# Kernel optimization log

Hardware: AMD Instinct MI355X
Metric: run time of the kernel (lower is better)

Reference implementation:

```python
import jax, jax.numpy as jnp
import numpy as np
import math

D_MODEL = 1024
N_HEAD = 16
D_HEAD = D_MODEL // N_HEAD


def setup_inputs() -> dict:
    key = jax.random.key(0)
    k0, k1, k2, k3, k4 = jax.random.split(key, 5)
    B, N = 4, 2048
    inp = jax.random.normal(k0, (B, N, D_MODEL), dtype=jnp.float32)
    # causal mask: True = keep (masked_fill on ~mask)
    mask = jnp.tril(jnp.ones((N, N), dtype=bool))
    # qkv_proj Linear(d_model, 3*d_model); output Linear(d_model, d_model)
    s_in = 1.0 / math.sqrt(D_MODEL)
    W_qkv = jax.random.uniform(k1, (D_MODEL, 3 * D_MODEL), jnp.float32, -s_in, s_in)
    b_qkv = jax.random.uniform(k2, (3 * D_MODEL,), jnp.float32, -s_in, s_in)
    W_out = jax.random.uniform(k3, (D_MODEL, D_MODEL), jnp.float32, -s_in, s_in)
    b_out = jax.random.uniform(k4, (D_MODEL,), jnp.float32, -s_in, s_in)
    return {"input": inp, "W_qkv": W_qkv, "b_qkv": b_qkv,
            "W_out": W_out, "b_out": b_out, "mask": mask}


def reference(input, W_qkv, b_qkv, W_out, b_out, mask):
    B, N, d = input.shape
    qkv = input @ W_qkv + b_qkv                       # [B,N,3d]  (dropout=eval no-op)
    q, k, v = jnp.split(qkv, 3, axis=-1)
    # [B,N,H,Dh] -> [B,H,N,Dh]
    q = q.reshape(B, N, N_HEAD, D_HEAD).transpose(0, 2, 1, 3)
    k = k.reshape(B, N, N_HEAD, D_HEAD).transpose(0, 2, 1, 3)
    v = v.reshape(B, N, N_HEAD, D_HEAD).transpose(0, 2, 1, 3)
    scale = 1.0 / math.sqrt(D_HEAD)
    scores = jnp.einsum('bhqd,bhkd->bhqk', q, k) * scale   # [B,H,N,N]
    scores = jnp.where(mask, scores, -jnp.inf)
    attn = jax.nn.softmax(scores, axis=-1)
    out = jnp.einsum('bhqk,bhkd->bhqd', attn, v)           # [B,H,N,Dh]
    out = out.transpose(0, 2, 1, 3).reshape(B, N, d)       # concat heads
    return out @ W_out + b_out
```

## Files before the change

kernel.cpp:

```cpp
#include <hip/hip_runtime.h>
#include <hip/hip_bf16.h>

typedef unsigned short u16;
typedef unsigned u32;
typedef __attribute__((ext_vector_type(4))) unsigned short u16x4;
typedef __attribute__((ext_vector_type(8))) unsigned short u16x8;
typedef __attribute__((ext_vector_type(4))) unsigned u32x4;
typedef __attribute__((ext_vector_type(8))) __bf16 bf16x8;
typedef __attribute__((ext_vector_type(4))) float f32x4;

typedef __attribute__((address_space(1))) void as1v;
typedef __attribute__((address_space(3))) void as3v;

#define MFMA16(a, b, c) __builtin_amdgcn_mfma_f32_16x16x32_bf16(a, b, c, 0, 0, 0)

__device__ __forceinline__ u16 f2bf(float f) {
    unsigned u = __builtin_bit_cast(unsigned, f);
    u += 0x7fffu + ((u >> 16) & 1u);
    return (u16)(u >> 16);
}

__device__ __forceinline__ u32 pkbf(float lo, float hi) {
    u32 r;
    asm("v_cvt_pk_bf16_f32 %0, %1, %2" : "=v"(r) : "v"(lo), "v"(hi));
    return r;
}

__device__ __forceinline__ void gload16(const void* g, void* l) {
    __builtin_amdgcn_global_load_lds((as1v*)g, (as3v*)l, 16, 0, 0);
}

__global__ void convert_f32_bf16(const float* __restrict__ in, u16* __restrict__ out, int n4) {
    int i = blockIdx.x * blockDim.x + threadIdx.x;
    if (i < n4) {
        float4 v = *(const float4*)&in[(size_t)i * 4];
        u16x4 o;
        o.x = f2bf(v.x); o.y = f2bf(v.y); o.z = f2bf(v.z); o.w = f2bf(v.w);
        *(u16x4*)&out[(size_t)i * 4] = o;
    }
}

__global__ void transpose_convert(const float* __restrict__ in, u16* __restrict__ out, int R, int C) {
    __shared__ float tl[64][65];
    const int rb = blockIdx.x, cb = blockIdx.y;
    const int tid = threadIdx.x;
    for (int it = 0; it < 4; ++it) {
        int lin = (tid + it * 256) * 4;
        int r = lin >> 6, c = lin & 63;
        float4 v = *(const float4*)&in[(size_t)(rb * 64 + r) * C + cb * 64 + c];
        tl[r][c + 0] = v.x; tl[r][c + 1] = v.y; tl[r][c + 2] = v.z; tl[r][c + 3] = v.w;
    }
    __syncthreads();
    for (int it = 0; it < 4; ++it) {
        int lin = (tid + it * 256) * 4;
        int oc = lin >> 6, orr = lin & 63;
        u16x4 o;
        o.x = f2bf(tl[orr + 0][oc]);
        o.y = f2bf(tl[orr + 1][oc]);
        o.z = f2bf(tl[orr + 2][oc]);
        o.w = f2bf(tl[orr + 3][oc]);
        *(u16x4*)&out[(size_t)(cb * 64 + oc) * R + rb * 64 + orr] = o;
    }
}

__global__ void transpose_v(const u16* __restrict__ vbuf, u16* __restrict__ vtb) {
    __shared__ u16 tl[64][65];
    const int nb = blockIdx.x, bh = blockIdx.y;
    const int tid = threadIdx.x;
    for (int it = 0; it < 2; ++it) {
        int lin = (tid + it * 256) * 8;
        int nl = lin >> 6, dh = lin & 63;
        u16x8 v = *(const u16x8*)&vbuf[((size_t)bh * 2048 + nb * 64 + nl) * 64 + dh];
#pragma unroll
        for (int j = 0; j < 8; ++j) tl[dh + j][nl] = v[j];
    }
    __syncthreads();
    for (int it = 0; it < 2; ++it) {
        int lin = (tid + it * 256) * 8;
        int dh = lin >> 6, nl = lin & 63;
        u16x8 o;
#pragma unroll
        for (int j = 0; j < 8; ++j) o[j] = tl[dh][nl + j];
        *(u16x8*)&vtb[((size_t)bh * 64 + dh) * 2048 + nb * 64 + nl] = o;
    }
}

__global__ __launch_bounds__(512, 2) void gemm256_qkv(
    const u16* __restrict__ A, const u16* __restrict__ Bt, const float* __restrict__ bias,
    u16* __restrict__ qb, u16* __restrict__ kb, u16* __restrict__ vb) {
    constexpr int K = 1024;
    constexpr int NT = 32;
    __shared__ u16 ldsu[65536];

    const int bid = blockIdx.x;
    const int swz = (bid & 7) * 48 + (bid >> 3);
    const int bm = swz / 12, bn = swz % 12;

    const int tid = threadIdx.x, wid = tid >> 6, lane = tid & 63;
    const int wr = wid >> 2, wc = wid & 3;
    const int l15 = lane & 15, lhi = lane >> 4;

    const int sslot = (lane & 7) ^ (lane >> 3);
    const int kcol = (sslot & 3) * 8;
    const int mloc = (lane >> 3) * 2 + (sslot >> 2);

    const u16* Arow[2];
    const u16* Brow[2];
#pragma unroll
    for (int li = 0; li < 2; ++li) {
        int sg = wid * 2 + li;
        int m = sg * 16 + mloc;
        Arow[li] = A + (size_t)(bm * 256 + m) * K + kcol;
        Brow[li] = Bt + (size_t)(bn * 256 + m) * K + kcol;
    }

    auto stageA = [&](int buf, int t) {
#pragma unroll
        for (int li = 0; li < 2; ++li) {
            int sg = wid * 2 + li;
            gload16(Arow[li] + t * 32, (char*)ldsu + buf * 32768 + sg * 1024);
        }
    };
    auto stageB = [&](int buf, int t) {
#pragma unroll
        for (int li = 0; li < 2; ++li) {
            int sg = wid * 2 + li;
            gload16(Brow[li] + t * 32, (char*)ldsu + buf * 32768 + 16384 + sg * 1024);
        }
    };

    const int rslot = ((l15 & 1) * 4 + lhi) ^ ((l15 >> 1) & 7);
    const int fragoff = (l15 >> 1) * 64 + rslot * 8;

    f32x4 acc[8][4];
#pragma unroll
    for (int i = 0; i < 8; ++i)
#pragma unroll
        for (int j = 0; j < 4; ++j) acc[i][j] = (f32x4){0.f, 0.f, 0.f, 0.f};

    auto doTile = [&](int cur, int tstage, bool dostage) {
        const u16* Ab = ldsu + cur * 16384 + wr * 4096 + fragoff;
        const u16* Bb = ldsu + cur * 16384 + 8192 + wc * 2048 + fragoff;
        bf16x8 af[8], b0, b1;
#pragma unroll
        for (int mf = 0; mf < 8; ++mf) af[mf] = *(const bf16x8*)(Ab + mf * 512);
        b0 = *(const bf16x8*)(Bb);
        b1 = *(const bf16x8*)(Bb + 512);
        if (dostage) stageA(tstage & 3, tstage);
        __builtin_amdgcn_s_setprio(1);
#pragma unroll
        for (int mf = 0; mf < 8; ++mf) {
            acc[mf][0] = MFMA16(af[mf], b0, acc[mf][0]);
            acc[mf][1] = MFMA16(af[mf], b1, acc[mf][1]);
        }
        __builtin_amdgcn_s_setprio(0);
        b0 = *(const bf16x8*)(Bb + 1024);
        b1 = *(const bf16x8*)(Bb + 1536);
        if (dostage) stageB(tstage & 3, tstage);
        __builtin_amdgcn_s_setprio(1);
#pragma unroll
        for (int mf = 0; mf < 8; ++mf) {
            acc[mf][2] = MFMA16(af[mf], b0, acc[mf][2]);
            acc[mf][3] = MFMA16(af[mf], b1, acc[mf][3]);
        }
        __builtin_amdgcn_s_setprio(0);
    };

    stageA(0, 0); stageB(0, 0);
    stageA(1, 1); stageB(1, 1);
    stageA(2, 2); stageB(2, 2);
    asm volatile("s_waitcnt vmcnt(8)" ::: "memory");
    __builtin_amdgcn_s_barrier();
    __builtin_amdgcn_sched_barrier(0);

    for (int t = 0; t < NT - 3; ++t) {
        doTile(t & 3, t + 3, true);
        asm volatile("s_waitcnt vmcnt(8)" ::: "memory");
        __builtin_amdgcn_s_barrier();
        __builtin_amdgcn_sched_barrier(0);
    }
    doTile((NT - 3) & 3, 0, false);
    asm volatile("s_waitcnt vmcnt(4)" ::: "memory");
    __builtin_amdgcn_s_barrier();
    __builtin_amdgcn_sched_barrier(0);
    doTile((NT - 2) & 3, 0, false);
    asm volatile("s_waitcnt vmcnt(0)" ::: "memory");
    __builtin_amdgcn_s_barrier();
    __builtin_amdgcn_sched_barrier(0);
    doTile((NT - 1) & 3, 0, false);

    const int bnbase = bn * 256 + wc * 64;
#pragma unroll
    for (int nf = 0; nf < 4; ++nf) {
        int cg = bnbase + nf * 16 + l15;
        float bv = bias[cg];
        int which = cg >> 10, rem = cg & 1023;
        u16* dst = (which == 0) ? qb : (which == 1) ? kb : vb;
        float qs = (which == 0) ? 0.18033688011112042f : 1.0f;
        size_t colterm = (size_t)(rem >> 6) * 131072 + (size_t)(rem & 63);
#pragma unroll
        for (int mf = 0; mf < 8; ++mf) {
            int rgb = bm * 256 + wr * 128 + mf * 16 + lhi * 4;
            size_t rowterm = (size_t)(rgb >> 11) * 2097152 + (size_t)(rgb & 2047) * 64;
#pragma unroll
            for (int v = 0; v < 4; ++v) {
                float val = (acc[mf][nf][v] + bv) * qs;
                dst[rowterm + (size_t)v * 64 + colterm] = f2bf(val);
            }
        }
    }
}

__global__ __launch_bounds__(256) void gemm_bt(
    const u16* __restrict__ A, const u16* __restrict__ Bt, const float* __restrict__ bias,
    int M, int N, int K, float* __restrict__ outf) {
    __shared__ u16 Al[128 * 32];
    __shared__ u16 Bl[128 * 32];
    const int bm = blockIdx.x, bn = blockIdx.y;
    const int tid = threadIdx.x, wid = tid >> 6, lane = tid & 63;
    const int wr = wid >> 1, wc = wid & 1;
    const int l15 = lane & 15, lhi = lane >> 4;

    f32x4 acc[4][4];
#pragma unroll
    for (int i = 0; i < 4; ++i)
#pragma unroll
        for (int j = 0; j < 4; ++j) acc[i][j] = (f32x4){0.f, 0.f, 0.f, 0.f};

    for (int k0 = 0; k0 < K; k0 += 32) {
        __syncthreads();
#pragma unroll
        for (int s = 0; s < 2; ++s) {
            int lin0 = (wid * 2 + s) * 1024;
            int off = lin0 + lane * 16;
            int row = off >> 6, colb = off & 63;
            const u16* ga = A + (size_t)(bm * 128 + row) * K + k0 + (colb >> 1);
            gload16(ga, (char*)Al + lin0);
            const u16* gb = Bt + (size_t)(bn * 128 + row) * K + k0 + (colb >> 1);
            gload16(gb, (char*)Bl + lin0);
        }
        __syncthreads();
        bf16x8 af[4], bfr[4];
#pragma unroll
        for (int mt = 0; mt < 4; ++mt)
            af[mt] = *(const bf16x8*)&Al[(wr * 64 + mt * 16 + l15) * 32 + lhi * 8];
#pragma unroll
        for (int nt = 0; nt < 4; ++nt)
            bfr[nt] = *(const bf16x8*)&Bl[(wc * 64 + nt * 16 + l15) * 32 + lhi * 8];
#pragma unroll
        for (int mt = 0; mt < 4; ++mt)
#pragma unroll
            for (int nt = 0; nt < 4; ++nt)
                acc[mt][nt] = MFMA16(af[mt], bfr[nt], acc[mt][nt]);
    }

#pragma unroll
    for (int mt = 0; mt < 4; ++mt)
#pragma unroll
        for (int nt = 0; nt < 4; ++nt)
#pragma unroll
            for (int v = 0; v < 4; ++v) {
                int rg = bm * 128 + wr * 64 + mt * 16 + lhi * 4 + v;
                int cg = bn * 128 + wc * 64 + nt * 16 + l15;
                outf[(size_t)rg * N + cg] = acc[mt][nt][v] + bias[cg];
            }
}

__global__ __launch_bounds__(256, 2) void attn_kernel(
    const u16* __restrict__ qbuf, const u16* __restrict__ kbuf,
    const u16* __restrict__ vtb, u16* __restrict__ obuf) {
    __shared__ u16 Kl[2][64 * 64];
    __shared__ u16 Vl[2][64 * 64];
    const int bid = blockIdx.x;
    const int c = (bid >> 3) & 7;
    const int bh = ((bid & 7) << 3) + (bid >> 6);
    const int b = bh >> 4, h = bh & 15;
    const int tid = threadIdx.x, wid = tid >> 6, lane = tid & 63;
    const int l15 = lane & 15, lhi = lane >> 4;
    const int qA0 = c * 128 + wid * 32;
    const int qB0 = (15 - c) * 128 + wid * 32;
    const int ntA = 2 * c + (wid >> 1) + 1;
    const int ntB = 31 - 2 * c + (wid >> 1);
    const int ntmax = 32 - 2 * c;

    auto loadQ = [&](int qbase, bf16x8* dst) {
        const u16* qp = qbuf + ((size_t)bh * 2048 + qbase + l15) * 64 + lhi * 8;
        dst[0] = *(const bf16x8*)(qp);
        dst[1] = *(const bf16x8*)(qp + 32);
    };
    bf16x8 qfA0[2], qfA1[2], qfB0[2], qfB1[2];
    loadQ(qA0, qfA0); loadQ(qA0 + 16, qfA1);
    loadQ(qB0, qfB0); loadQ(qB0 + 16, qfB1);

    float mA0 = -1e30f, lA0 = 0.f, mA1 = -1e30f, lA1 = 0.f;
    float mB0 = -1e30f, lB0 = 0.f, mB1 = -1e30f, lB1 = 0.f;
    f32x4 oA0[4], oA1[4], oB0[4], oB1[4];
#pragma unroll
    for (int d = 0; d < 4; ++d) {
        oA0[d] = (f32x4){0.f, 0.f, 0.f, 0.f}; oA1[d] = (f32x4){0.f, 0.f, 0.f, 0.f};
        oB0[d] = (f32x4){0.f, 0.f, 0.f, 0.f}; oB1[d] = (f32x4){0.f, 0.f, 0.f, 0.f};
    }

    const int srow = lane >> 3;
    const int scolb = ((lane & 7) * 16) ^ (srow << 4);

    auto stage = [&](int buf, int t) {
        const int kbase = t * 64;
#pragma unroll
        for (int s = 0; s < 2; ++s) {
            int sg = wid * 2 + s;
            int row = sg * 8 + srow;
            const u16* gk = kbuf + ((size_t)bh * 2048 + kbase + row) * 64 + (scolb >> 1);
            gload16(gk, (char*)Kl[buf] + sg * 1024);
            const u16* gv = vtb + ((size_t)bh * 64 + row) * 2048 + kbase + (scolb >> 1);
            gload16(gv, (char*)Vl[buf] + sg * 1024);
        }
    };

    auto smax = [&](f32x4* s, int qg0, int t, float& m, float& l, f32x4* oa, u32* pw) {
        const int qg = qg0 + l15;
        if (64 * t + 63 > qg0) {
#pragma unroll
            for (int kb4 = 0; kb4 < 4; ++kb4)
#pragma unroll
                for (int v = 0; v < 4; ++v) {
                    int kg = 64 * t + kb4 * 16 + lhi * 4 + v;
                    if (kg > qg) s[kb4][v] = -1e30f;
                }
        }
        float pm = fmaxf(fmaxf(fmaxf(s[0][0], s[0][1]), fmaxf(s[0][2], s[0][3])),
                         fmaxf(fmaxf(s[1][0], s[1][1]), fmaxf(s[1][2], s[1][3])));
        pm = fmaxf(pm, fmaxf(fmaxf(fmaxf(s[2][0], s[2][1]), fmaxf(s[2][2], s[2][3])),
                             fmaxf(fmaxf(s[3][0], s[3][1]), fmaxf(s[3][2], s[3][3]))));
        pm = fmaxf(pm, __shfl_xor(pm, 16, 64));
        pm = fmaxf(pm, __shfl_xor(pm, 32, 64));
        if (!__all(pm <= m + 8.f)) {
            float nm = fmaxf(m, pm);
            float f = exp2f(m - nm);
            m = nm;
            l *= f;
#pragma unroll
            for (int d = 0; d < 4; ++d)
#pragma unroll
                for (int v = 0; v < 4; ++v) oa[d][v] *= f;
        }
        float rs = 0.f;
#pragma unroll
        for (int kb4 = 0; kb4 < 4; ++kb4)
#pragma unroll
            for (int v = 0; v < 4; ++v) {
                float e = exp2f(s[kb4][v] - m);
                s[kb4][v] = e;
                rs += e;
            }
        rs += __shfl_xor(rs, 16, 64);
        rs += __shfl_xor(rs, 32, 64);
        l += rs;
        pw[0] = pkbf(s[0][0], s[0][1]); pw[1] = pkbf(s[0][2], s[0][3]);
        pw[2] = pkbf(s[1][0], s[1][1]); pw[3] = pkbf(s[1][2], s[1][3]);
        pw[4] = pkbf(s[2][0], s[2][1]); pw[5] = pkbf(s[2][2], s[2][3]);
        pw[6] = pkbf(s[3][0], s[3][1]); pw[7] = pkbf(s[3][2], s[3][3]);
    };

    auto computeChunk = [&](const char* Kb, const char* Vb, int t, int q0,
                            const bf16x8* qf0, const bf16x8* qf1,
                            float& m0, float& l0, f32x4* oa0,
                            float& m1, float& l1, f32x4* oa1) {
        f32x4 s0[4], s1[4];
        __builtin_amdgcn_s_setprio(1);
#pragma unroll
        for (int kb4 = 0; kb4 < 4; ++kb4) {
            const int r = kb4 * 16 + l15;
            const int sw = (r & 7) << 4;
            const int rowb = r * 128;
            bf16x8 kf0 = *(const bf16x8*)(Kb + rowb + ((lhi * 16) ^ sw));
            bf16x8 kf1 = *(const bf16x8*)(Kb + rowb + ((64 + lhi * 16) ^ sw));
            f32x4 a0 = (f32x4){0.f, 0.f, 0.f, 0.f};
            a0 = MFMA16(kf0, qf0[0], a0);
            a0 = MFMA16(kf1, qf0[1], a0);
            s0[kb4] = a0;
            f32x4 a1 = (f32x4){0.f, 0.f, 0.f, 0.f};
            a1 = MFMA16(kf0, qf1[0], a1);
            a1 = MFMA16(kf1, qf1[1], a1);
            s1[kb4] = a1;
        }
        __builtin_amdgcn_s_setprio(0);
        u32 pw0[8], pw1[8];
        smax(s0, q0, t, m0, l0, oa0, pw0);
        smax(s1, q0 + 16, t, m1, l1, oa1, pw1);
        __builtin_amdgcn_s_setprio(1);
#pragma unroll
        for (int ks = 0; ks < 2; ++ks) {
            bf16x8 pb0 = __builtin_bit_cast(bf16x8,
                (u32x4){pw0[ks * 4 + 0], pw0[ks * 4 + 1], pw0[ks * 4 + 2], pw0[ks * 4 + 3]});
            bf16x8 pb1 = __builtin_bit_cast(bf16x8,
                (u32x4){pw1[ks * 4 + 0], pw1[ks * 4 + 1], pw1[ks * 4 + 2], pw1[ks * 4 + 3]});
#pragma unroll
            for (int dhb = 0; dhb < 4; ++dhb) {
                const int r = dhb * 16 + l15;
                const int sw = (r & 7) << 4;
                u16x4 v0 = *(const u16x4*)(Vb + r * 128 + ((ks * 64 + 8 * lhi) ^ sw));
                u16x4 v1 = *(const u16x4*)(Vb + r * 128 + ((ks * 64 + 32 + 8 * lhi) ^ sw));
                u16x8 vv = {v0[0], v0[1], v0[2], v0[3], v1[0], v1[1], v1[2], v1[3]};
                bf16x8 vf = __builtin_bit_cast(bf16x8, vv);
                oa0[dhb] = MFMA16(vf, pb0, oa0[dhb]);
                oa1[dhb] = MFMA16(vf, pb1, oa1[dhb]);
            }
        }
        __builtin_amdgcn_s_setprio(0);
    };

    auto step = [&](const char* Kb, const char* Vb, int t) {
        if (t < ntB) computeChunk(Kb, Vb, t, qB0, qfB0, qfB1, mB0, lB0, oB0, mB1, lB1, oB1);
        if (t < ntA) computeChunk(Kb, Vb, t, qA0, qfA0, qfA1, mA0, lA0, oA0, mA1, lA1, oA1);
    };

    stage(0, 0);
    int t = 0;
    for (;;) {
        __syncthreads();
        if (t + 1 < ntmax) stage(1, t + 1);
        step((const char*)Kl[0], (const char*)Vl[0], t);
        if (++t == ntmax) break;
        __syncthreads();
        if (t + 1 < ntmax) stage(0, t + 1);
        step((const char*)Kl[1], (const char*)Vl[1], t);
        if (++t == ntmax) break;
    }

    auto epi = [&](int q0, float l, const f32x4* oa) {
        const float rl = 1.f / l;
        const int q = q0 + l15;
        const size_t rowoff = ((size_t)b * 2048 + q) * 1024 + h * 64;
#pragma unroll
        for (int dhb = 0; dhb < 4; ++dhb) {
            u16x4 w;
#pragma unroll
            for (int v = 0; v < 4; ++v) w[v] = f2bf(oa[dhb][v] * rl);
            *(u16x4*)&obuf[rowoff + dhb * 16 + lhi * 4] = w;
        }
    };
    epi(qA0, lA0, oA0);
    epi(qA0 + 16, lA1, oA1);
    epi(qB0, lB0, oB0);
    epi(qB0 + 16, lB1, oB1);
}

extern "C" void kernel_launch(void* const* d_in, const int* in_sizes, int n_in,
                              void* d_out, int out_size, void* d_ws, size_t ws_size,
                              hipStream_t stream) {
    const float* inp   = (const float*)d_in[0];
    const float* W_qkv = (const float*)d_in[1];
    const float* b_qkv = (const float*)d_in[2];
    const float* W_out = (const float*)d_in[3];
    const float* b_out = (const float*)d_in[4];
    float* out = (float*)d_out;

    u16* xb   = (u16*)d_ws;
    u16* wqt  = xb + 8388608;
    u16* wot  = wqt + 3145728;
    u16* qbuf = wot + 1048576;
    u16* kbuf = qbuf + 8388608;
    u16* vbuf = kbuf + 8388608;
    u16* vtb  = vbuf + 8388608;
    u16* obuf = vtb + 8388608;

    convert_f32_bf16<<<8192, 256, 0, stream>>>(inp, xb, 2097152);
    transpose_convert<<<dim3(16, 48), 256, 0, stream>>>(W_qkv, wqt, 1024, 3072);
    transpose_convert<<<dim3(16, 16), 256, 0, stream>>>(W_out, wot, 1024, 1024);
    gemm256_qkv<<<384, 512, 0, stream>>>(xb, wqt, b_qkv, qbuf, kbuf, vbuf);
    transpose_v<<<dim3(32, 64), 256, 0, stream>>>(vbuf, vtb);
    attn_kernel<<<512, 256, 0, stream>>>(qbuf, kbuf, vtb, obuf);
    gemm_bt<<<dim3(64, 8), 256, 0, stream>>>(obuf, wot, b_out, 8192, 1024, 1024, out);
}
```

Measured before the change: 203.1 us.

## Split paired causal query tiles into separate blocks, heaviest first

Each attention block previously handled two mirrored 128-row query tiles (c and 15-c) so that causal work was balanced per block. Now each block handles a single query tile, the grid doubles to 1024 blocks, and block IDs are ordered so the longest tiles (largest c) are dispatched first. Register use per block roughly halves, so launch bounds rise to 4 blocks per CU for higher occupancy. In exchange, K/V tiles are no longer shared between the two query tiles, so K/V staging traffic per unit of work rises, and load balance now depends on the hardware scheduler.

```diff
diff --git a/kernel.cpp b/kernel.cpp
--- a/kernel.cpp
+++ b/kernel.cpp
@@ -266,39 +266,36 @@
             }
 }
 
-__global__ __launch_bounds__(256, 2) void attn_kernel(
+__global__ __launch_bounds__(256, 4) void attn_kernel(
     const u16* __restrict__ qbuf, const u16* __restrict__ kbuf,
     const u16* __restrict__ vtb, u16* __restrict__ obuf) {
     __shared__ u16 Kl[2][64 * 64];
     __shared__ u16 Vl[2][64 * 64];
     const int bid = blockIdx.x;
-    const int c = (bid >> 3) & 7;
-    const int bh = ((bid & 7) << 3) + (bid >> 6);
+    const int idx = bid >> 3;
+    const int c = 15 - (idx >> 3);
+    const int bh = ((bid & 7) << 3) + (idx & 7);
     const int b = bh >> 4, h = bh & 15;
     const int tid = threadIdx.x, wid = tid >> 6, lane = tid & 63;
     const int l15 = lane & 15, lhi = lane >> 4;
-    const int qA0 = c * 128 + wid * 32;
-    const int qB0 = (15 - c) * 128 + wid * 32;
-    const int ntA = 2 * c + (wid >> 1) + 1;
-    const int ntB = 31 - 2 * c + (wid >> 1);
-    const int ntmax = 32 - 2 * c;
+    const int q0 = c * 128 + wid * 32;
+    const int ntW = 2 * c + (wid >> 1) + 1;
+    const int ntmax = 2 * c + 2;
 
     auto loadQ = [&](int qbase, bf16x8* dst) {
         const u16* qp = qbuf + ((size_t)bh * 2048 + qbase + l15) * 64 + lhi * 8;
         dst[0] = *(const bf16x8*)(qp);
         dst[1] = *(const bf16x8*)(qp + 32);
     };
-    bf16x8 qfA0[2], qfA1[2], qfB0[2], qfB1[2];
-    loadQ(qA0, qfA0); loadQ(qA0 + 16, qfA1);
-    loadQ(qB0, qfB0); loadQ(qB0 + 16, qfB1);
-
-    float mA0 = -1e30f, lA0 = 0.f, mA1 = -1e30f, lA1 = 0.f;
-    float mB0 = -1e30f, lB0 = 0.f, mB1 = -1e30f, lB1 = 0.f;
-    f32x4 oA0[4], oA1[4], oB0[4], oB1[4];
+    bf16x8 qf0[2], qf1[2];
+    loadQ(q0, qf0); loadQ(q0 + 16, qf1);
+
+    float m0 = -1e30f, l0 = 0.f, m1 = -1e30f, l1 = 0.f;
+    f32x4 o0[4], o1[4];
 #pragma unroll
     for (int d = 0; d < 4; ++d) {
-        oA0[d] = (f32x4){0.f, 0.f, 0.f, 0.f}; oA1[d] = (f32x4){0.f, 0.f, 0.f, 0.f};
-        oB0[d] = (f32x4){0.f, 0.f, 0.f, 0.f}; oB1[d] = (f32x4){0.f, 0.f, 0.f, 0.f};
+        o0[d] = (f32x4){0.f, 0.f, 0.f, 0.f};
+        o1[d] = (f32x4){0.f, 0.f, 0.f, 0.f};
     }
 
     const int srow = lane >> 3;
@@ -362,10 +359,7 @@
         pw[6] = pkbf(s[3][0], s[3][1]); pw[7] = pkbf(s[3][2], s[3][3]);
     };
 
-    auto computeChunk = [&](const char* Kb, const char* Vb, int t, int q0,
-                            const bf16x8* qf0, const bf16x8* qf1,
-                            float& m0, float& l0, f32x4* oa0,
-                            float& m1, float& l1, f32x4* oa1) {
+    auto computeChunk = [&](const char* Kb, const char* Vb, int t) {
         f32x4 s0[4], s1[4];
         __builtin_amdgcn_s_setprio(1);
 #pragma unroll
@@ -386,8 +380,8 @@
         }
         __builtin_amdgcn_s_setprio(0);
         u32 pw0[8], pw1[8];
-        smax(s0, q0, t, m0, l0, oa0, pw0);
-        smax(s1, q0 + 16, t, m1, l1, oa1, pw1);
+        smax(s0, q0, t, m0, l0, o0, pw0);
+        smax(s1, q0 + 16, t, m1, l1, o1, pw1);
         __builtin_amdgcn_s_setprio(1);
 #pragma unroll
         for (int ks = 0; ks < 2; ++ks) {
@@ -403,16 +397,11 @@
                 u16x4 v1 = *(const u16x4*)(Vb + r * 128 + ((ks * 64 + 32 + 8 * lhi) ^ sw));
                 u16x8 vv = {v0[0], v0[1], v0[2], v0[3], v1[0], v1[1], v1[2], v1[3]};
                 bf16x8 vf = __builtin_bit_cast(bf16x8, vv);
-                oa0[dhb] = MFMA16(vf, pb0, oa0[dhb]);
-                oa1[dhb] = MFMA16(vf, pb1, oa1[dhb]);
+                o0[dhb] = MFMA16(vf, pb0, o0[dhb]);
+                o1[dhb] = MFMA16(vf, pb1, o1[dhb]);
             }
         }
         __builtin_amdgcn_s_setprio(0);
-    };
-
-    auto step = [&](const char* Kb, const char* Vb, int t) {
-        if (t < ntB) computeChunk(Kb, Vb, t, qB0, qfB0, qfB1, mB0, lB0, oB0, mB1, lB1, oB1);
-        if (t < ntA) computeChunk(Kb, Vb, t, qA0, qfA0, qfA1, mA0, lA0, oA0, mA1, lA1, oA1);
     };
 
     stage(0, 0);
@@ -420,17 +409,17 @@
     for (;;) {
         __syncthreads();
         if (t + 1 < ntmax) stage(1, t + 1);
-        step((const char*)Kl[0], (const char*)Vl[0], t);
+        if (t < ntW) computeChunk((const char*)Kl[0], (const char*)Vl[0], t);
         if (++t == ntmax) break;
         __syncthreads();
         if (t + 1 < ntmax) stage(0, t + 1);
-        step((const char*)Kl[1], (const char*)Vl[1], t);
+        if (t < ntW) computeChunk((const char*)Kl[1], (const char*)Vl[1], t);
         if (++t == ntmax) break;
     }
 
-    auto epi = [&](int q0, float l, const f32x4* oa) {
+    auto epi = [&](int qg0, float l, const f32x4* oa) {
         const float rl = 1.f / l;
-        const int q = q0 + l15;
+        const int q = qg0 + l15;
         const size_t rowoff = ((size_t)b * 2048 + q) * 1024 + h * 64;
 #pragma unroll
         for (int dhb = 0; dhb < 4; ++dhb) {
@@ -440,10 +429,8 @@
             *(u16x4*)&obuf[rowoff + dhb * 16 + lhi * 4] = w;
         }
     };
-    epi(qA0, lA0, oA0);
-    epi(qA0 + 16, lA1, oA1);
-    epi(qB0, lB0, oB0);
-    epi(qB0 + 16, lB1, oB1);
+    epi(q0, l0, o0);
+    epi(q0 + 16, l1, o1);
 }
 
 extern "C" void kernel_launch(void* const* d_in, const int* in_sizes, int n_in,
@@ -470,6 +457,6 @@
     transpose_convert<<<dim3(16, 16), 256, 0, stream>>>(W_out, wot, 1024, 1024);
     gemm256_qkv<<<384, 512, 0, stream>>>(xb, wqt, b_qkv, qbuf, kbuf, vbuf);
     transpose_v<<<dim3(32, 64), 256, 0, stream>>>(vbuf, vtb);
-    attn_kernel<<<512, 256, 0, stream>>>(qbuf, kbuf, vtb, obuf);
+    attn_kernel<<<1024, 256, 0, stream>>>(qbuf, kbuf, vtb, obuf);
     gemm_bt<<<dim3(64, 8), 256, 0, stream>>>(obuf, wot, b_out, 8192, 1024, 1024, out);
 }
```

Result: faster. 192.0 us (-5.5%).
